# Optimization experiments

Hardware: AMD Instinct MI355X
Metric: run time of the kernel (lower is better)

## Reference

```python
import jax, jax.numpy as jnp
import numpy as np

CUTOFF = 5.0
N = 8192
BOX = 55.0


def setup_inputs() -> dict:
    key = jax.random.key(0)
    xyz = jax.random.uniform(key, (N, 3), dtype=jnp.float32) * BOX
    cell = jnp.diag(jnp.full((3,), BOX, dtype=jnp.float32))  # [3,3] box vectors (rows)
    ii, jj = np.triu_indices(N, k=1)  # all i<j candidate pairs, P = N*(N-1)/2
    return {
        "xyz": xyz,
        "cell": cell,
        "idx_i": jnp.asarray(ii, dtype=jnp.int32),
        "idx_j": jnp.asarray(jj, dtype=jnp.int32),
    }


def _min_image_deltas(xyz, cell, idx_i, idx_j):
    # [P,3] raw displacement for every candidate pair
    delta = xyz[idx_i] - xyz[idx_j]
    # triclinic minimum-image reduction, z -> y -> x order (NNPOps convention)
    delta = delta - jnp.round(delta[:, 2:3] / cell[2, 2]) * cell[2]
    delta = delta - jnp.round(delta[:, 1:2] / cell[1, 1]) * cell[1]
    delta = delta - jnp.round(delta[:, 0:1] / cell[0, 0]) * cell[0]
    dist = jnp.sqrt(jnp.sum(delta * delta, axis=1))  # [P]
    return delta, dist


def reference(xyz, cell, idx_i, idx_j):
    delta, dist = _min_image_deltas(xyz, cell, idx_i, idx_j)
    mask = dist < CUTOFF  # [P] bool
    # neighbors: -1 marks pairs beyond cutoff (fixed-shape output, jit-safe)
    pair_i = jnp.where(mask, idx_i, jnp.int32(-1))
    pair_j = jnp.where(mask, idx_j, jnp.int32(-1))
    pair_diff = jnp.where(mask[:, None], delta, jnp.float32(0.0))  # [P,3]
    pair_dist = jnp.where(mask, dist, jnp.float32(0.0))  # [P]
    return pair_i, pair_j, pair_diff, pair_dist
```

## Files before the change

### kernel.cpp

```cpp
#include <hip/hip_runtime.h>
#include <math.h>


#define NL_CUTOFF 5.0f

__device__ __forceinline__ void solve_ij(int p, int N, int& io, int& jo) {
    const int A = 2 * N - 1;
    const int disc = A * A - 8 * p;
    const float sd = __fsqrt_rn((float)disc);
    int ii = (int)(__fmul_rn(__fsub_rn((float)A, sd), 0.5f));
    if (ii < 0) ii = 0;
    if (ii > N - 2) ii = N - 2;
    while (ii > 0 && ((ii * (A - ii)) >> 1) > p) --ii;
    while ((((ii + 1) * (A - ii - 1)) >> 1) <= p) ++ii;
    io = ii;
    jo = p - ((ii * (A - ii)) >> 1) + ii + 1;
}

struct CellC {
    float r0x, r0y, r0z, rc0;
    float r1x, r1y, r1z, rc1;
    float r2x, r2y, r2z, rc2;
};

template <bool DIAG>
__device__ __forceinline__ void pair_compute(
    float xi, float yi, float zi, float xj, float yj, float zj,
    const CellC& c, float fi, float fj,
    float& oi, float& oj, float& odx, float& ody, float& odz, float& orr)
{
    float dx = __fsub_rn(xi, xj);
    float dy = __fsub_rn(yi, yj);
    float dz = __fsub_rn(zi, zj);

    if (DIAG) {
        float s = rintf(__fmul_rn(dz, c.rc2));
        dz = __fsub_rn(dz, __fmul_rn(s, c.r2z));
        s = rintf(__fmul_rn(dy, c.rc1));
        dy = __fsub_rn(dy, __fmul_rn(s, c.r1y));
        s = rintf(__fmul_rn(dx, c.rc0));
        dx = __fsub_rn(dx, __fmul_rn(s, c.r0x));
    } else {
        float s = rintf(__fmul_rn(dz, c.rc2));
        dx = __fsub_rn(dx, __fmul_rn(s, c.r2x));
        dy = __fsub_rn(dy, __fmul_rn(s, c.r2y));
        dz = __fsub_rn(dz, __fmul_rn(s, c.r2z));

        s = rintf(__fmul_rn(dy, c.rc1));
        dx = __fsub_rn(dx, __fmul_rn(s, c.r1x));
        dy = __fsub_rn(dy, __fmul_rn(s, c.r1y));
        dz = __fsub_rn(dz, __fmul_rn(s, c.r1z));

        s = rintf(__fmul_rn(dx, c.rc0));
        dx = __fsub_rn(dx, __fmul_rn(s, c.r0x));
        dy = __fsub_rn(dy, __fmul_rn(s, c.r0y));
        dz = __fsub_rn(dz, __fmul_rn(s, c.r0z));
    }

    float ss = __fadd_rn(__fadd_rn(__fmul_rn(dx, dx), __fmul_rn(dy, dy)),
                         __fmul_rn(dz, dz));
    float r = __fsqrt_rn(ss);
    bool m = (r < NL_CUTOFF);

    oi  = m ? fi : -1.0f;
    oj  = m ? fj : -1.0f;
    odx = m ? dx : 0.0f;
    ody = m ? dy : 0.0f;
    odz = m ? dz : 0.0f;
    orr = m ? r  : 0.0f;
}

template <bool DIAG>
__device__ __forceinline__ void nl_body(
    const float* __restrict__ xyz, const CellC& c,
    float* __restrict__ out, long long P, int N)
{
    float* __restrict__ out_i = out;
    float* __restrict__ out_j = out + P;
    float* __restrict__ out_d = out + 2 * P;
    float* __restrict__ out_r = out + 5 * P;

    const long long nquad  = P >> 2;
    const long long stride = (long long)gridDim.x * blockDim.x;
    const long long tid0   = (long long)blockIdx.x * blockDim.x + threadIdx.x;

    for (long long q = tid0; q < nquad; q += stride) {
        int i, j;
        solve_ij((int)(q << 2), N, i, j);

        float oia[4], oja[4], ora[4], od[12];
        if (j + 3 <= N - 1) {
            const float xi = xyz[3 * i + 0], yi = xyz[3 * i + 1], zi = xyz[3 * i + 2];
            const float fi = (float)i, fj = (float)j;
#pragma unroll
            for (int k = 0; k < 4; ++k) {
                pair_compute<DIAG>(xi, yi, zi,
                                   xyz[3 * (j + k) + 0], xyz[3 * (j + k) + 1],
                                   xyz[3 * (j + k) + 2],
                                   c, fi, fj + (float)k,
                                   oia[k], oja[k], od[3 * k + 0], od[3 * k + 1],
                                   od[3 * k + 2], ora[k]);
            }
        } else {
            int ii = i, jj = j;
#pragma unroll
            for (int k = 0; k < 4; ++k) {
                pair_compute<DIAG>(xyz[3 * ii + 0], xyz[3 * ii + 1], xyz[3 * ii + 2],
                                   xyz[3 * jj + 0], xyz[3 * jj + 1], xyz[3 * jj + 2],
                                   c, (float)ii, (float)jj,
                                   oia[k], oja[k], od[3 * k + 0], od[3 * k + 1],
                                   od[3 * k + 2], ora[k]);
                if (++jj >= N) { ++ii; jj = ii + 1; }
            }
        }

        ((float4*)out_i)[q] = make_float4(oia[0], oia[1], oia[2], oia[3]);
        ((float4*)out_j)[q] = make_float4(oja[0], oja[1], oja[2], oja[3]);
        ((float4*)out_r)[q] = make_float4(ora[0], ora[1], ora[2], ora[3]);
        float4* dd = (float4*)(out_d + 12 * q);
        dd[0] = make_float4(od[0], od[1],  od[2],  od[3]);
        dd[1] = make_float4(od[4], od[5],  od[6],  od[7]);
        dd[2] = make_float4(od[8], od[9],  od[10], od[11]);
    }

    for (long long p = (nquad << 2) + tid0; p < P; p += stride) {
        int i, j;
        solve_ij((int)p, N, i, j);
        float oi, oj, dx, dy, dz, rr;
        pair_compute<DIAG>(xyz[3 * i + 0], xyz[3 * i + 1], xyz[3 * i + 2],
                           xyz[3 * j + 0], xyz[3 * j + 1], xyz[3 * j + 2],
                           c, (float)i, (float)j, oi, oj, dx, dy, dz, rr);
        out_i[p] = oi;
        out_j[p] = oj;
        out_d[3 * p + 0] = dx;
        out_d[3 * p + 1] = dy;
        out_d[3 * p + 2] = dz;
        out_r[p] = rr;
    }
}

__global__ __launch_bounds__(256) void nl_kernel(
    const float* __restrict__ xyz,
    const float* __restrict__ cell,
    float* __restrict__ out,
    long long P, int N)
{
    CellC c;
    c.r0x = cell[0]; c.r0y = cell[1]; c.r0z = cell[2];
    c.r1x = cell[3]; c.r1y = cell[4]; c.r1z = cell[5];
    c.r2x = cell[6]; c.r2y = cell[7]; c.r2z = cell[8];
    c.rc0 = __fdiv_rn(1.0f, c.r0x);
    c.rc1 = __fdiv_rn(1.0f, c.r1y);
    c.rc2 = __fdiv_rn(1.0f, c.r2z);

    const bool diag = (c.r0y == 0.0f) && (c.r0z == 0.0f) &&
                      (c.r1x == 0.0f) && (c.r1z == 0.0f) &&
                      (c.r2x == 0.0f) && (c.r2y == 0.0f);

    if (diag) nl_body<true>(xyz, c, out, P, N);
    else      nl_body<false>(xyz, c, out, P, N);
}

extern "C" void kernel_launch(void* const* d_in, const int* in_sizes, int n_in,
                              void* d_out, int out_size, void* d_ws, size_t ws_size,
                              hipStream_t stream) {
    const float* xyz  = (const float*)d_in[0];
    const float* cell = (const float*)d_in[1];
    float* out = (float*)d_out;

    const int       N = in_sizes[0] / 3;
    const long long P = (long long)in_sizes[2];

    const int block = 256;
    long long nquad = P >> 2;
    long long blocks_needed = (nquad + block - 1) / block;
    int grid = (int)(blocks_needed < 2048 ? (blocks_needed > 0 ? blocks_needed : 1)
                                          : 2048);

    nl_kernel<<<grid, block, 0, stream>>>(xyz, cell, out, P, N);
}
```

Before: 165.7 us.

## Recompute pair values per output stream so each pass writes one contiguous array

Each block now owns a fixed contiguous range of 4096 quads and runs four passes over it. Each pass recomputes the pair values and writes only one output array (i, j, r, then the deltas), so a wavefront's stores go to one region at a time instead of four. The j coordinates are now fetched with three 16-byte vector loads, and the launch bound asks for 8 blocks per SM. This costs about four times the compute and index solving, and it relies on the vector loads staying in bounds near the end of xyz.

```diff
diff --git a/kernel.cpp b/kernel.cpp
--- a/kernel.cpp
+++ b/kernel.cpp
@@ -3,6 +3,10 @@
 
 
 #define NL_CUTOFF 5.0f
+#define QPB 4096
+#define BLOCK 256
+
+typedef float f32x4 __attribute__((ext_vector_type(4)));
 
 __device__ __forceinline__ void solve_ij(int p, int N, int& io, int& jo) {
     const int A = 2 * N - 1;
@@ -71,6 +75,47 @@
 }
 
 template <bool DIAG>
+__device__ __forceinline__ void quad_vals(
+    const float* __restrict__ xyz, const CellC& c, long long q, int N,
+    float* oia, float* oja, float* ora, float* od)
+{
+    int i, j;
+    solve_ij((int)(q << 2), N, i, j);
+
+    if (j + 3 <= N - 1) {
+        const float xi = xyz[3 * i + 0], yi = xyz[3 * i + 1], zi = xyz[3 * i + 2];
+        const float fi = (float)i, fj = (float)j;
+
+        const float* jb = xyz + 3 * j;
+        f32x4 va, vb, vc;
+        __builtin_memcpy(&va, jb + 0, 16);
+        __builtin_memcpy(&vb, jb + 4, 16);
+        __builtin_memcpy(&vc, jb + 8, 16);
+        const float jx[4] = {va.x, va.w, vb.z, vc.y};
+        const float jy[4] = {va.y, vb.x, vb.w, vc.z};
+        const float jz[4] = {va.z, vb.y, vc.x, vc.w};
+#pragma unroll
+        for (int k = 0; k < 4; ++k) {
+            pair_compute<DIAG>(xi, yi, zi, jx[k], jy[k], jz[k],
+                               c, fi, fj + (float)k,
+                               oia[k], oja[k], od[3 * k + 0], od[3 * k + 1],
+                               od[3 * k + 2], ora[k]);
+        }
+    } else {
+        int ii = i, jj = j;
+#pragma unroll
+        for (int k = 0; k < 4; ++k) {
+            pair_compute<DIAG>(xyz[3 * ii + 0], xyz[3 * ii + 1], xyz[3 * ii + 2],
+                               xyz[3 * jj + 0], xyz[3 * jj + 1], xyz[3 * jj + 2],
+                               c, (float)ii, (float)jj,
+                               oia[k], oja[k], od[3 * k + 0], od[3 * k + 1],
+                               od[3 * k + 2], ora[k]);
+            if (++jj >= N) { ++ii; jj = ii + 1; }
+        }
+    }
+}
+
+template <bool DIAG>
 __device__ __forceinline__ void nl_body(
     const float* __restrict__ xyz, const CellC& c,
     float* __restrict__ out, long long P, int N)
@@ -80,66 +125,59 @@
     float* __restrict__ out_d = out + 2 * P;
     float* __restrict__ out_r = out + 5 * P;
 
-    const long long nquad  = P >> 2;
-    const long long stride = (long long)gridDim.x * blockDim.x;
-    const long long tid0   = (long long)blockIdx.x * blockDim.x + threadIdx.x;
-
-    for (long long q = tid0; q < nquad; q += stride) {
-        int i, j;
-        solve_ij((int)(q << 2), N, i, j);
-
-        float oia[4], oja[4], ora[4], od[12];
-        if (j + 3 <= N - 1) {
-            const float xi = xyz[3 * i + 0], yi = xyz[3 * i + 1], zi = xyz[3 * i + 2];
-            const float fi = (float)i, fj = (float)j;
-#pragma unroll
-            for (int k = 0; k < 4; ++k) {
-                pair_compute<DIAG>(xi, yi, zi,
-                                   xyz[3 * (j + k) + 0], xyz[3 * (j + k) + 1],
-                                   xyz[3 * (j + k) + 2],
-                                   c, fi, fj + (float)k,
-                                   oia[k], oja[k], od[3 * k + 0], od[3 * k + 1],
-                                   od[3 * k + 2], ora[k]);
-            }
-        } else {
-            int ii = i, jj = j;
-#pragma unroll
-            for (int k = 0; k < 4; ++k) {
-                pair_compute<DIAG>(xyz[3 * ii + 0], xyz[3 * ii + 1], xyz[3 * ii + 2],
-                                   xyz[3 * jj + 0], xyz[3 * jj + 1], xyz[3 * jj + 2],
-                                   c, (float)ii, (float)jj,
-                                   oia[k], oja[k], od[3 * k + 0], od[3 * k + 1],
-                                   od[3 * k + 2], ora[k]);
-                if (++jj >= N) { ++ii; jj = ii + 1; }
-            }
-        }
-
+    const long long nquad = P >> 2;
+    const long long qbase = (long long)blockIdx.x * QPB;
+    const int       tid   = (int)threadIdx.x;
+
+    float oia[4], oja[4], ora[4], od[12];
+
+    for (int it = 0; it < QPB / BLOCK; ++it) {
+        const long long q = qbase + it * BLOCK + tid;
+        if (q >= nquad) break;
+        quad_vals<DIAG>(xyz, c, q, N, oia, oja, ora, od);
         ((float4*)out_i)[q] = make_float4(oia[0], oia[1], oia[2], oia[3]);
+    }
+    for (int it = 0; it < QPB / BLOCK; ++it) {
+        const long long q = qbase + it * BLOCK + tid;
+        if (q >= nquad) break;
+        quad_vals<DIAG>(xyz, c, q, N, oia, oja, ora, od);
         ((float4*)out_j)[q] = make_float4(oja[0], oja[1], oja[2], oja[3]);
+    }
+    for (int it = 0; it < QPB / BLOCK; ++it) {
+        const long long q = qbase + it * BLOCK + tid;
+        if (q >= nquad) break;
+        quad_vals<DIAG>(xyz, c, q, N, oia, oja, ora, od);
         ((float4*)out_r)[q] = make_float4(ora[0], ora[1], ora[2], ora[3]);
+    }
+    for (int it = 0; it < QPB / BLOCK; ++it) {
+        const long long q = qbase + it * BLOCK + tid;
+        if (q >= nquad) break;
+        quad_vals<DIAG>(xyz, c, q, N, oia, oja, ora, od);
         float4* dd = (float4*)(out_d + 12 * q);
         dd[0] = make_float4(od[0], od[1],  od[2],  od[3]);
         dd[1] = make_float4(od[4], od[5],  od[6],  od[7]);
         dd[2] = make_float4(od[8], od[9],  od[10], od[11]);
     }
 
-    for (long long p = (nquad << 2) + tid0; p < P; p += stride) {
-        int i, j;
-        solve_ij((int)p, N, i, j);
-        float oi, oj, dx, dy, dz, rr;
-        pair_compute<DIAG>(xyz[3 * i + 0], xyz[3 * i + 1], xyz[3 * i + 2],
-                           xyz[3 * j + 0], xyz[3 * j + 1], xyz[3 * j + 2],
-                           c, (float)i, (float)j, oi, oj, dx, dy, dz, rr);
-        out_i[p] = oi;
-        out_j[p] = oj;
-        out_d[3 * p + 0] = dx;
-        out_d[3 * p + 1] = dy;
-        out_d[3 * p + 2] = dz;
-        out_r[p] = rr;
-    }
-}
-
-__global__ __launch_bounds__(256) void nl_kernel(
+    if (blockIdx.x == 0) {
+        for (long long p = (nquad << 2) + tid; p < P; p += BLOCK) {
+            int i, j;
+            solve_ij((int)p, N, i, j);
+            float oi, oj, dx, dy, dz, rr;
+            pair_compute<DIAG>(xyz[3 * i + 0], xyz[3 * i + 1], xyz[3 * i + 2],
+                               xyz[3 * j + 0], xyz[3 * j + 1], xyz[3 * j + 2],
+                               c, (float)i, (float)j, oi, oj, dx, dy, dz, rr);
+            out_i[p] = oi;
+            out_j[p] = oj;
+            out_d[3 * p + 0] = dx;
+            out_d[3 * p + 1] = dy;
+            out_d[3 * p + 2] = dz;
+            out_r[p] = rr;
+        }
+    }
+}
+
+__global__ __launch_bounds__(256, 8) void nl_kernel(
     const float* __restrict__ xyz,
     const float* __restrict__ cell,
     float* __restrict__ out,
@@ -171,11 +209,9 @@
     const int       N = in_sizes[0] / 3;
     const long long P = (long long)in_sizes[2];
 
-    const int block = 256;
-    long long nquad = P >> 2;
-    long long blocks_needed = (nquad + block - 1) / block;
-    int grid = (int)(blocks_needed < 2048 ? (blocks_needed > 0 ? blocks_needed : 1)
-                                          : 2048);
-
-    nl_kernel<<<grid, block, 0, stream>>>(xyz, cell, out, P, N);
-}
+    const long long nquad = P >> 2;
+    int grid = (int)((nquad + QPB - 1) / QPB);
+    if (grid < 1) grid = 1;
+
+    nl_kernel<<<grid, BLOCK, 0, stream>>>(xyz, cell, out, P, N);
+}
```

New measurement: 256.7 us. 54.9% more time.
